# Optimization experiments

Hardware: AMD Instinct MI355X
Metric: run time of the kernel (lower is better)

## Reference

```python
import jax, jax.numpy as jnp
import numpy as np

DIM = 1024
HEADS = 16
HEAD_DIM = DIM // HEADS


def setup_inputs() -> dict:
    key = jax.random.key(0)
    ks = jax.random.split(key, 5)
    s = 1.0 / np.sqrt(DIM)
    x = jax.random.normal(ks[0], (2, 2048, DIM), dtype=jnp.float32)
    # torch nn.Linear weights are [out_features, in_features]
    W_qkv = jax.random.uniform(ks[1], (3 * DIM, DIM), dtype=jnp.float32, minval=-s, maxval=s)
    b_qkv = jax.random.uniform(ks[2], (3 * DIM,), dtype=jnp.float32, minval=-s, maxval=s)
    W_out = jax.random.uniform(ks[3], (DIM, DIM), dtype=jnp.float32, minval=-s, maxval=s)
    b_out = jax.random.uniform(ks[4], (DIM,), dtype=jnp.float32, minval=-s, maxval=s)
    return {"x": x, "W_qkv": W_qkv, "b_qkv": b_qkv, "W_out": W_out, "b_out": b_out}


def reference(x, W_qkv, b_qkv, W_out, b_out):
    B, N, D = x.shape
    qkv = jnp.einsum('bnd,ed->bne', x, W_qkv) + b_qkv            # [B,N,3D]
    qkv = qkv.reshape(B, N, 3, HEADS, HEAD_DIM)
    qkv = jnp.transpose(qkv, (2, 0, 3, 1, 4))                    # [3,B,H,N,hd]
    q, k, v = qkv[0], qkv[1], qkv[2]
    scale = 1.0 / np.sqrt(HEAD_DIM).astype(np.float32)
    attn = jnp.einsum('bhnd,bhmd->bhnm', q, k) * scale           # [B,H,N,N]
    attn = jax.nn.softmax(attn, axis=-1)
    out = jnp.einsum('bhnm,bhmd->bhnd', attn, v)                 # [B,H,N,hd]
    out = jnp.transpose(out, (0, 2, 1, 3)).reshape(B, N, D)
    out = jnp.einsum('bnd,ed->bne', out, W_out) + b_out
    return out
```

## Files before the change

kernel.cpp:

```cpp
#include <hip/hip_runtime.h>
#include <stdint.h>
#include <stddef.h>

typedef __attribute__((ext_vector_type(4))) float  f32x4;
typedef __attribute__((ext_vector_type(8))) short  s16x8;
typedef __attribute__((ext_vector_type(4))) float  float4v;
typedef __attribute__((ext_vector_type(4))) unsigned short u16x4;
typedef __attribute__((ext_vector_type(2))) unsigned int   u32x2;

#define DIM    1024
#define HEADS  16
#define HD     64
#define SEQ    2048
#define BATCH  2
#define TOKENS (BATCH * SEQ)

#define QSCALE 0.18033688011112042f

__device__ __forceinline__ unsigned short f2bf(float f) {
  union { float f; uint32_t u; } x; x.f = f;
  uint32_t r = x.u + 0x7fffu + ((x.u >> 16) & 1u);
  return (unsigned short)(r >> 16);
}

__device__ __forceinline__ float fast_exp2(float x) {
#if __has_builtin(__builtin_amdgcn_exp2f)
  return __builtin_amdgcn_exp2f(x);
#else
  return exp2f(x);
#endif
}

__device__ __forceinline__ uint32_t pack_bf16_trunc(uint32_t lo, uint32_t hi) {
#if __has_builtin(__builtin_amdgcn_perm)
  return __builtin_amdgcn_perm(hi, lo, 0x07060302u);
#else
  return (hi & 0xffff0000u) | (lo >> 16);
#endif
}

__device__ __forceinline__ void stage16(const unsigned short* gp, unsigned short* lp) {
#if __has_builtin(__builtin_amdgcn_global_load_lds)
  __builtin_amdgcn_global_load_lds((const __attribute__((address_space(1))) void*)gp,
                                   (__attribute__((address_space(3))) void*)lp, 16, 0, 0);
#else
  *(s16x8*)(lp + (threadIdx.x & 63) * 8) = *(const s16x8*)gp;
#endif
}

#define N4_X  (TOKENS * DIM / 4)
#define N4_WQ (3 * DIM * DIM / 4)
#define N4_WO (DIM * DIM / 4)
__global__ __launch_bounds__(256) void mhsa_cast_all(const float* __restrict__ x,
    const float* __restrict__ wq, const float* __restrict__ wo,
    unsigned short* __restrict__ xb, unsigned short* __restrict__ wqb,
    unsigned short* __restrict__ wob) {
  int i = blockIdx.x * 256 + threadIdx.x;
  const float* src; unsigned short* dst; int off;
  if (i < N4_X)              { src = x;  dst = xb;  off = i; }
  else if (i < N4_X + N4_WQ) { src = wq; dst = wqb; off = i - N4_X; }
  else                       { src = wo; dst = wob; off = i - (N4_X + N4_WQ); }
  float4v f = ((const float4v*)src)[off];
  u16x4 o;
  o.x = f2bf(f.x); o.y = f2bf(f.y); o.z = f2bf(f.z); o.w = f2bf(f.w);
  ((u16x4*)dst)[off] = o;
}


__global__ __launch_bounds__(256, 3) void mhsa_gemm_qkv(const unsigned short* __restrict__ A,
    const unsigned short* __restrict__ Bw, const float* __restrict__ bias,
    unsigned short* __restrict__ qws, unsigned short* __restrict__ kws,
    unsigned short* __restrict__ vws) {
  __shared__ unsigned short As[2][128 * 32];
  __shared__ unsigned short Bs[2][128 * 32];
  const int t = threadIdx.x;
  const int w = t >> 6, l = t & 63;
  const int wm = w >> 1, wn = w & 1;
  const int rowBase = blockIdx.y * 128;
  const int colBase = blockIdx.x * 128;
  const int fr = l & 15, q4 = l >> 4, ln = l & 15;
  const int srow = l >> 2;
  const int scol = ((l & 3) ^ (srow & 3)) * 8;

  f32x4 zero = {0.f, 0.f, 0.f, 0.f};
  f32x4 acc[4][4];
  #pragma unroll
  for (int a = 0; a < 4; ++a)
    #pragma unroll
    for (int b = 0; b < 4; ++b) acc[a][b] = zero;

  #pragma unroll
  for (int it = 0; it < 2; ++it) {
    const int c = w * 2 + it;
    stage16(A  + (size_t)(rowBase + c * 16 + srow) * DIM + scol, &As[0][c * 512]);
    stage16(Bw + (size_t)(colBase + c * 16 + srow) * DIM + scol, &Bs[0][c * 512]);
  }
  __syncthreads();

  for (int kt = 0; kt < DIM / 32; ++kt) {
    const int cur = kt & 1, nxt = cur ^ 1;
    if (kt + 1 < DIM / 32) {
      const int k1 = (kt + 1) * 32;
      #pragma unroll
      for (int it = 0; it < 2; ++it) {
        const int c = w * 2 + it;
        stage16(A  + (size_t)(rowBase + c * 16 + srow) * DIM + k1 + scol, &As[nxt][c * 512]);
        stage16(Bw + (size_t)(colBase + c * 16 + srow) * DIM + k1 + scol, &Bs[nxt][c * 512]);
      }
    }
    s16x8 xf[4], wf[4];
    #pragma unroll
    for (int b = 0; b < 4; ++b)
      xf[b] = *(const s16x8*)&As[cur][(wm * 64 + b * 16 + fr) * 32 + ((q4 ^ (fr & 3)) * 8)];
    #pragma unroll
    for (int a = 0; a < 4; ++a)
      wf[a] = *(const s16x8*)&Bs[cur][(wn * 64 + a * 16 + fr) * 32 + ((q4 ^ (fr & 3)) * 8)];
    #pragma unroll
    for (int a = 0; a < 4; ++a)
      #pragma unroll
      for (int b = 0; b < 4; ++b)
        acc[a][b] = __builtin_amdgcn_mfma_f32_16x16x32_bf16(wf[a], xf[b], acc[a][b], 0, 0, 0);
    __syncthreads();
  }

  const int which = colBase >> 10;
  const float sc = (which == 0) ? QSCALE : 1.0f;
  unsigned short* dst = (which == 0) ? qws : ((which == 1) ? kws : vws);

  #pragma unroll
  for (int a = 0; a < 4; ++a) {
    const int e0 = colBase + wn * 64 + a * 16 + q4 * 4;
    const float4v bs4 = *(const float4v*)&bias[e0];
    const int rr0 = e0 & 1023;
    const int h = rr0 >> 6, d0 = rr0 & 63;
    #pragma unroll
    for (int b = 0; b < 4; ++b) {
      const int tok = rowBase + wm * 64 + b * 16 + ln;
      const int bb = tok >> 11, n = tok & 2047;
      if (which != 2) {
        u16x4 pk;
        #pragma unroll
        for (int r = 0; r < 4; ++r) pk[r] = f2bf((acc[a][b][r] + bs4[r]) * sc);
        *(u16x4*)&dst[(((size_t)(bb * HEADS + h)) * SEQ + n) * HD + d0] = pk;
      } else {
        #pragma unroll
        for (int r = 0; r < 4; ++r)
          dst[(((size_t)(bb * HEADS + h)) * HD + d0 + r) * SEQ + n] =
              f2bf(acc[a][b][r] + bs4[r]);
      }
    }
  }
}

__global__ __launch_bounds__(256, 3) void mhsa_gemm_out(const unsigned short* __restrict__ A,
    const unsigned short* __restrict__ Bw, const float* __restrict__ bias,
    float* __restrict__ out) {
  __shared__ unsigned short As[2][64 * 32];
  __shared__ unsigned short Bs[2][128 * 32];
  const int t = threadIdx.x;
  const int w = t >> 6, l = t & 63;
  const int wm = w >> 1, wn = w & 1;
  const int rowBase = blockIdx.y * 64;
  const int colBase = blockIdx.x * 128;
  const int fr = l & 15, q4 = l >> 4, ln = l & 15;
  const int srow = l >> 2;
  const int scol = ((l & 3) ^ (srow & 3)) * 8;

  f32x4 zero = {0.f, 0.f, 0.f, 0.f};
  f32x4 acc[4][2];
  #pragma unroll
  for (int a = 0; a < 4; ++a)
    #pragma unroll
    for (int b = 0; b < 2; ++b) acc[a][b] = zero;

  #pragma unroll
  for (int it = 0; it < 3; ++it) {
    const int s = w * 3 + it;
    if (s < 4) stage16(A  + (size_t)(rowBase + s * 16 + srow) * DIM + scol, &As[0][s * 512]);
    else       stage16(Bw + (size_t)(colBase + (s - 4) * 16 + srow) * DIM + scol, &Bs[0][(s - 4) * 512]);
  }
  __syncthreads();

  for (int kt = 0; kt < DIM / 32; ++kt) {
    const int cur = kt & 1, nxt = cur ^ 1;
    if (kt + 1 < DIM / 32) {
      const int k1 = (kt + 1) * 32;
      #pragma unroll
      for (int it = 0; it < 3; ++it) {
        const int s = w * 3 + it;
        if (s < 4) stage16(A  + (size_t)(rowBase + s * 16 + srow) * DIM + k1 + scol, &As[nxt][s * 512]);
        else       stage16(Bw + (size_t)(colBase + (s - 4) * 16 + srow) * DIM + k1 + scol, &Bs[nxt][(s - 4) * 512]);
      }
    }
    s16x8 xf[2], wf[4];
    #pragma unroll
    for (int b = 0; b < 2; ++b)
      xf[b] = *(const s16x8*)&As[cur][(wm * 32 + b * 16 + fr) * 32 + ((q4 ^ (fr & 3)) * 8)];
    #pragma unroll
    for (int a = 0; a < 4; ++a)
      wf[a] = *(const s16x8*)&Bs[cur][(wn * 64 + a * 16 + fr) * 32 + ((q4 ^ (fr & 3)) * 8)];
    #pragma unroll
    for (int a = 0; a < 4; ++a)
      #pragma unroll
      for (int b = 0; b < 2; ++b)
        acc[a][b] = __builtin_amdgcn_mfma_f32_16x16x32_bf16(wf[a], xf[b], acc[a][b], 0, 0, 0);
    __syncthreads();
  }

  #pragma unroll
  for (int a = 0; a < 4; ++a) {
    const int e0 = colBase + wn * 64 + a * 16 + q4 * 4;
    const float4v bs4 = *(const float4v*)&bias[e0];
    #pragma unroll
    for (int b = 0; b < 2; ++b) {
      const int tok = rowBase + wm * 32 + b * 16 + ln;
      float4v v;
      #pragma unroll
      for (int r = 0; r < 4; ++r) v[r] = acc[a][b][r] + bs4[r];
      *(float4v*)&out[(size_t)tok * DIM + e0] = v;
    }
  }
}

__global__ __launch_bounds__(256, 2) void mhsa_attn(const unsigned short* __restrict__ q,
    const unsigned short* __restrict__ k, const unsigned short* __restrict__ vt,
    unsigned short* __restrict__ o) {
  __shared__ unsigned short QPs[4 * 32 * 72];
  __shared__ unsigned short Ks[2][64 * 64];
  __shared__ unsigned short Vs[2][64 * 64];
  const int t = threadIdx.x, w = t >> 6, l = t & 63;
  const int q4 = l >> 4, ln = l & 15;
  const int bh = blockIdx.y, q0 = blockIdx.x * 128;
  const unsigned short* qb  = q  + (size_t)bh * SEQ * HD;
  const unsigned short* kb  = k  + (size_t)bh * SEQ * HD;
  const unsigned short* vtb = vt + (size_t)bh * HD * SEQ;

  const int srow = l >> 3;
  const int scol = ((l & 7) ^ srow) * 8;

  unsigned short* Pw = &QPs[w * (32 * 72)];

  #pragma unroll
  for (int it = 0; it < 4; ++it)
    stage16(qb + (size_t)(q0 + w * 32 + it * 8 + srow) * HD + scol, &Pw[it * 512]);
  #pragma unroll
  for (int it = 0; it < 2; ++it) {
    const int c = w + it * 4;
    stage16(kb  + (size_t)(c * 8 + srow) * HD + scol,        &Ks[0][c * 512]);
    stage16(vtb + (size_t)(c * 8 + srow) * SEQ + scol,       &Vs[0][c * 512]);
    stage16(kb  + (size_t)(64 + c * 8 + srow) * HD + scol,   &Ks[1][c * 512]);
  }
  __syncthreads();

  s16x8 aq[2][2];
  #pragma unroll
  for (int i = 0; i < 2; ++i)
    #pragma unroll
    for (int kk = 0; kk < 2; ++kk)
      aq[i][kk] = *(const s16x8*)&Pw[(i * 16 + ln) * 64 + (((kk * 4 + q4) ^ (ln & 7)) * 8)];

  f32x4 zero = {0.f, 0.f, 0.f, 0.f};
  f32x4 accO[2][4];
  float lsum[2] = {0.f, 0.f};
  #pragma unroll
  for (int i = 0; i < 2; ++i)
    #pragma unroll
    for (int jd = 0; jd < 4; ++jd) accO[i][jd] = zero;

  {
    f32x4 St[4][2];
    #pragma unroll
    for (int jb = 0; jb < 4; ++jb)
      #pragma unroll
      for (int i = 0; i < 2; ++i) St[jb][i] = zero;
    #pragma unroll
    for (int jb = 0; jb < 4; ++jb) {
      s16x8 ak0 = *(const s16x8*)&Ks[0][(jb * 16 + ln) * 64 + ((q4 ^ (ln & 7)) * 8)];
      s16x8 ak1 = *(const s16x8*)&Ks[0][(jb * 16 + ln) * 64 + (((4 + q4) ^ (ln & 7)) * 8)];
      #pragma unroll
      for (int i = 0; i < 2; ++i) {
        St[jb][i] = __builtin_amdgcn_mfma_f32_16x16x32_bf16(ak0, aq[i][0], St[jb][i], 0, 0, 0);
        St[jb][i] = __builtin_amdgcn_mfma_f32_16x16x32_bf16(ak1, aq[i][1], St[jb][i], 0, 0, 0);
      }
    }
    #pragma unroll
    for (int i = 0; i < 2; ++i)
      #pragma unroll
      for (int jb = 0; jb < 4; ++jb) {
        uint32_t u0 = __float_as_uint(fast_exp2(St[jb][i][0]));
        uint32_t u1 = __float_as_uint(fast_exp2(St[jb][i][1]));
        uint32_t u2 = __float_as_uint(fast_exp2(St[jb][i][2]));
        uint32_t u3 = __float_as_uint(fast_exp2(St[jb][i][3]));
        lsum[i] += __uint_as_float(u0 & 0xffff0000u) + __uint_as_float(u1 & 0xffff0000u)
                 + __uint_as_float(u2 & 0xffff0000u) + __uint_as_float(u3 & 0xffff0000u);
        u32x2 pk;
        pk.x = pack_bf16_trunc(u0, u1);
        pk.y = pack_bf16_trunc(u2, u3);
        *(u32x2*)&Pw[(i * 16 + ln) * 72 + jb * 16 + q4 * 4] = pk;
      }
  }
  __syncthreads();

  const int NT = SEQ / 64;
  for (int jt = 0; jt < NT; ++jt) {
    const int cur = jt & 1, nxt = cur ^ 1;
    if (jt + 2 < NT) {
      const int j2 = (jt + 2) * 64;
      #pragma unroll
      for (int it = 0; it < 2; ++it) {
        const int c = w + it * 4;
        stage16(kb + (size_t)(j2 + c * 8 + srow) * HD + scol, &Ks[cur][c * 512]);
      }
    }
    if (jt + 1 < NT) {
      const int j1 = (jt + 1) * 64;
      #pragma unroll
      for (int it = 0; it < 2; ++it) {
        const int c = w + it * 4;
        stage16(vtb + (size_t)(c * 8 + srow) * SEQ + j1 + scol, &Vs[nxt][c * 512]);
      }
    }

    s16x8 ap[2][2];
    #pragma unroll
    for (int i = 0; i < 2; ++i)
      #pragma unroll
      for (int kk = 0; kk < 2; ++kk)
        ap[i][kk] = *(const s16x8*)&Pw[(i * 16 + ln) * 72 + kk * 32 + q4 * 8];

    if (jt + 1 < NT) {
      f32x4 St[4][2];
      #pragma unroll
      for (int jb = 0; jb < 4; ++jb)
        #pragma unroll
        for (int i = 0; i < 2; ++i) St[jb][i] = zero;
      #pragma unroll
      for (int jb = 0; jb < 4; ++jb) {
        s16x8 ak0 = *(const s16x8*)&Ks[nxt][(jb * 16 + ln) * 64 + ((q4 ^ (ln & 7)) * 8)];
        s16x8 ak1 = *(const s16x8*)&Ks[nxt][(jb * 16 + ln) * 64 + (((4 + q4) ^ (ln & 7)) * 8)];
        #pragma unroll
        for (int i = 0; i < 2; ++i) {
          St[jb][i] = __builtin_amdgcn_mfma_f32_16x16x32_bf16(ak0, aq[i][0], St[jb][i], 0, 0, 0);
          St[jb][i] = __builtin_amdgcn_mfma_f32_16x16x32_bf16(ak1, aq[i][1], St[jb][i], 0, 0, 0);
        }
      }

      #pragma unroll
      for (int jd = 0; jd < 4; ++jd) {
        s16x8 bv0 = *(const s16x8*)&Vs[cur][(jd * 16 + ln) * 64 + ((q4 ^ (ln & 7)) * 8)];
        s16x8 bv1 = *(const s16x8*)&Vs[cur][(jd * 16 + ln) * 64 + (((4 + q4) ^ (ln & 7)) * 8)];
        #pragma unroll
        for (int i = 0; i < 2; ++i) {
          accO[i][jd] = __builtin_amdgcn_mfma_f32_16x16x32_bf16(ap[i][0], bv0, accO[i][jd], 0, 0, 0);
          accO[i][jd] = __builtin_amdgcn_mfma_f32_16x16x32_bf16(ap[i][1], bv1, accO[i][jd], 0, 0, 0);
        }
      }

      #pragma unroll
      for (int i = 0; i < 2; ++i)
        #pragma unroll
        for (int jb = 0; jb < 4; ++jb) {
          uint32_t u0 = __float_as_uint(fast_exp2(St[jb][i][0]));
          uint32_t u1 = __float_as_uint(fast_exp2(St[jb][i][1]));
          uint32_t u2 = __float_as_uint(fast_exp2(St[jb][i][2]));
          uint32_t u3 = __float_as_uint(fast_exp2(St[jb][i][3]));
          lsum[i] += __uint_as_float(u0 & 0xffff0000u) + __uint_as_float(u1 & 0xffff0000u)
                   + __uint_as_float(u2 & 0xffff0000u) + __uint_as_float(u3 & 0xffff0000u);
          u32x2 pk;
          pk.x = pack_bf16_trunc(u0, u1);
          pk.y = pack_bf16_trunc(u2, u3);
          *(u32x2*)&Pw[(i * 16 + ln) * 72 + jb * 16 + q4 * 4] = pk;
        }
    } else {
      #pragma unroll
      for (int jd = 0; jd < 4; ++jd) {
        s16x8 bv0 = *(const s16x8*)&Vs[cur][(jd * 16 + ln) * 64 + ((q4 ^ (ln & 7)) * 8)];
        s16x8 bv1 = *(const s16x8*)&Vs[cur][(jd * 16 + ln) * 64 + (((4 + q4) ^ (ln & 7)) * 8)];
        #pragma unroll
        for (int i = 0; i < 2; ++i) {
          accO[i][jd] = __builtin_amdgcn_mfma_f32_16x16x32_bf16(ap[i][0], bv0, accO[i][jd], 0, 0, 0);
          accO[i][jd] = __builtin_amdgcn_mfma_f32_16x16x32_bf16(ap[i][1], bv1, accO[i][jd], 0, 0, 0);
        }
      }
    }

    __syncthreads();
  }

  const int b = bh >> 4, h = bh & 15;
  #pragma unroll
  for (int i = 0; i < 2; ++i) {
    float s = lsum[i];
    s += __shfl_xor(s, 16);
    s += __shfl_xor(s, 32);
    const float inv = 1.f / s;
    #pragma unroll
    for (int r = 0; r < 4; ++r) {
      const float invr = __shfl(inv, (l & 48) + q4 * 4 + r);
      const int row = q0 + w * 32 + i * 16 + q4 * 4 + r;
      #pragma unroll
      for (int jd = 0; jd < 4; ++jd)
        o[((size_t)(b * SEQ + row)) * DIM + h * HD + jd * 16 + ln] = f2bf(accO[i][jd][r] * invr);
    }
  }
}

extern "C" void kernel_launch(void* const* d_in, const int* in_sizes, int n_in,
                              void* d_out, int out_size, void* d_ws, size_t ws_size,
                              hipStream_t stream) {
  const float* x     = (const float*)d_in[0];
  const float* Wqkv  = (const float*)d_in[1];
  const float* bqkv  = (const float*)d_in[2];
  const float* Wout  = (const float*)d_in[3];
  const float* bout  = (const float*)d_in[4];
  float* out = (float*)d_out;

  unsigned short* ws = (unsigned short*)d_ws;
  unsigned short* x_bf    = ws;
  unsigned short* wqkv_bf = x_bf    + (size_t)TOKENS * DIM;
  unsigned short* wout_bf = wqkv_bf + (size_t)3 * DIM * DIM;
  unsigned short* q_ws    = wout_bf + (size_t)DIM * DIM;
  unsigned short* k_ws    = q_ws    + (size_t)TOKENS * DIM;
  unsigned short* v_ws    = k_ws    + (size_t)TOKENS * DIM;
  unsigned short* ao_ws   = v_ws    + (size_t)TOKENS * DIM;

  {
    const int n4 = N4_X + N4_WQ + N4_WO;
    mhsa_cast_all<<<n4 / 256, 256, 0, stream>>>(x, Wqkv, Wout, x_bf, wqkv_bf, wout_bf);
  }

  {
    dim3 grid(3 * DIM / 128, TOKENS / 128);
    mhsa_gemm_qkv<<<grid, 256, 0, stream>>>(x_bf, wqkv_bf, bqkv, q_ws, k_ws, v_ws);
  }

  {
    dim3 grid(SEQ / 128, BATCH * HEADS);
    mhsa_attn<<<grid, 256, 0, stream>>>(q_ws, k_ws, v_ws, ao_ws);
  }

  {
    dim3 grid(DIM / 128, TOKENS / 64);
    mhsa_gemm_out<<<grid, 256, 0, stream>>>(ao_ws, wout_bf, bout, out);
  }
}
```

Baseline: 193.1 us.

## Store Q/K/V in MFMA fragment order and load fragments directly from global

The QKV projection epilogue now writes Q, K and V in a pre-swizzled layout that matches the MFMA operand fragments. The attention kernel can then load each lane's 8-element fragment straight from global memory into registers. This drops the shared-memory staging of K and V and the per-tile __syncthreads, with register double-buffering of K and V fragments replacing the LDS double-buffering. The cost is higher register pressure from 64 extra VGPRs of fragment buffers. It also relies on L2/global latency being hidden without LDS reuse, since each wave reloads K/V independently (four waves read the same data), and the V epilogue now uses scattered 2-byte stores.

```diff
diff --git a/kernel.cpp b/kernel.cpp
--- a/kernel.cpp
+++ b/kernel.cpp
@@ -124,29 +124,47 @@
   }
 
   const int which = colBase >> 10;
-  const float sc = (which == 0) ? QSCALE : 1.0f;
-  unsigned short* dst = (which == 0) ? qws : ((which == 1) ? kws : vws);
-
-  #pragma unroll
-  for (int a = 0; a < 4; ++a) {
-    const int e0 = colBase + wn * 64 + a * 16 + q4 * 4;
-    const float4v bs4 = *(const float4v*)&bias[e0];
-    const int rr0 = e0 & 1023;
-    const int h = rr0 >> 6, d0 = rr0 & 63;
-    #pragma unroll
-    for (int b = 0; b < 4; ++b) {
-      const int tok = rowBase + wm * 64 + b * 16 + ln;
-      const int bb = tok >> 11, n = tok & 2047;
-      if (which != 2) {
+  if (which != 2) {
+    unsigned short* dst = (which == 0) ? qws : kws;
+    const float sc = (which == 0) ? QSCALE : 1.0f;
+    #pragma unroll
+    for (int a = 0; a < 4; ++a) {
+      const int e0 = colBase + wn * 64 + a * 16 + q4 * 4;
+      const float4v bs4 = *(const float4v*)&bias[e0];
+      const int h = (e0 & 1023) >> 6;
+      const int kkf = a >> 1;
+      const int q4s = ((a & 1) << 1) | (q4 >> 1);
+      const int jf  = (q4 & 1) * 4;
+      #pragma unroll
+      for (int b = 0; b < 4; ++b) {
+        const int tok = rowBase + wm * 64 + b * 16 + ln;
+        const int bb = tok >> 11, n = tok & 2047;
+        const int bhl = bb * HEADS + h;
         u16x4 pk;
         #pragma unroll
         for (int r = 0; r < 4; ++r) pk[r] = f2bf((acc[a][b][r] + bs4[r]) * sc);
-        *(u16x4*)&dst[(((size_t)(bb * HEADS + h)) * SEQ + n) * HD + d0] = pk;
-      } else {
+        const size_t off = ((size_t)(bhl * (SEQ / 16) + (n >> 4)) * 2 + kkf) * 512
+                         + q4s * 128 + ln * 8 + jf;
+        *(u16x4*)&dst[off] = pk;
+      }
+    }
+  } else {
+    #pragma unroll
+    for (int a = 0; a < 4; ++a) {
+      const int e0 = colBase + wn * 64 + a * 16 + q4 * 4;
+      const float4v bs4 = *(const float4v*)&bias[e0];
+      const int h = (e0 & 1023) >> 6;
+      #pragma unroll
+      for (int b = 0; b < 4; ++b) {
+        const int tok = rowBase + wm * 64 + b * 16 + ln;
+        const int bb = tok >> 11, n = tok & 2047;
+        const int bhl = bb * HEADS + h;
+        const int kt = n >> 6, kkf = (n >> 5) & 1, q4s = (n >> 3) & 3, jf = n & 7;
+        const size_t base = ((size_t)((bhl * (SEQ / 64) + kt) * 8 + a * 2 + kkf)) * 512
+                          + q4s * 128 + jf;
         #pragma unroll
         for (int r = 0; r < 4; ++r)
-          dst[(((size_t)(bb * HEADS + h)) * HD + d0 + r) * SEQ + n] =
-              f2bf(acc[a][b][r] + bs4[r]);
+          vws[base + (q4 * 4 + r) * 8] = f2bf(acc[a][b][r] + bs4[r]);
       }
     }
   }
@@ -222,42 +240,24 @@
   }
 }
 
-__global__ __launch_bounds__(256, 2) void mhsa_attn(const unsigned short* __restrict__ q,
-    const unsigned short* __restrict__ k, const unsigned short* __restrict__ vt,
+__global__ __launch_bounds__(256, 2) void mhsa_attn(const unsigned short* __restrict__ qF,
+    const unsigned short* __restrict__ kF, const unsigned short* __restrict__ vF,
     unsigned short* __restrict__ o) {
-  __shared__ unsigned short QPs[4 * 32 * 72];
-  __shared__ unsigned short Ks[2][64 * 64];
-  __shared__ unsigned short Vs[2][64 * 64];
+  __shared__ unsigned short Ps[4 * 32 * 72];
   const int t = threadIdx.x, w = t >> 6, l = t & 63;
   const int q4 = l >> 4, ln = l & 15;
   const int bh = blockIdx.y, q0 = blockIdx.x * 128;
-  const unsigned short* qb  = q  + (size_t)bh * SEQ * HD;
-  const unsigned short* kb  = k  + (size_t)bh * SEQ * HD;
-  const unsigned short* vtb = vt + (size_t)bh * HD * SEQ;
-
-  const int srow = l >> 3;
-  const int scol = ((l & 7) ^ srow) * 8;
-
-  unsigned short* Pw = &QPs[w * (32 * 72)];
-
-  #pragma unroll
-  for (int it = 0; it < 4; ++it)
-    stage16(qb + (size_t)(q0 + w * 32 + it * 8 + srow) * HD + scol, &Pw[it * 512]);
-  #pragma unroll
-  for (int it = 0; it < 2; ++it) {
-    const int c = w + it * 4;
-    stage16(kb  + (size_t)(c * 8 + srow) * HD + scol,        &Ks[0][c * 512]);
-    stage16(vtb + (size_t)(c * 8 + srow) * SEQ + scol,       &Vs[0][c * 512]);
-    stage16(kb  + (size_t)(64 + c * 8 + srow) * HD + scol,   &Ks[1][c * 512]);
-  }
-  __syncthreads();
+  const unsigned short* qb = qF + (size_t)bh * (SEQ * HD);
+  const unsigned short* kb = kF + (size_t)bh * (SEQ * HD);
+  const unsigned short* vb = vF + (size_t)bh * (SEQ * HD);
+  unsigned short* Pw = &Ps[w * (32 * 72)];
 
   s16x8 aq[2][2];
   #pragma unroll
   for (int i = 0; i < 2; ++i)
     #pragma unroll
     for (int kk = 0; kk < 2; ++kk)
-      aq[i][kk] = *(const s16x8*)&Pw[(i * 16 + ln) * 64 + (((kk * 4 + q4) ^ (ln & 7)) * 8)];
+      aq[i][kk] = *(const s16x8*)&qb[((size_t)((q0 >> 4) + w * 2 + i) * 2 + kk) * 512 + l * 8];
 
   f32x4 zero = {0.f, 0.f, 0.f, 0.f};
   f32x4 accO[2][4];
@@ -267,6 +267,17 @@
     #pragma unroll
     for (int jd = 0; jd < 4; ++jd) accO[i][jd] = zero;
 
+  s16x8 kfr[2][4][2], vfr[2][4][2];
+
+  #pragma unroll
+  for (int jb = 0; jb < 4; ++jb)
+    #pragma unroll
+    for (int kk = 0; kk < 2; ++kk) {
+      kfr[1][jb][kk] = *(const s16x8*)&kb[(size_t)((jb * 2 + kk)) * 512 + l * 8];
+      vfr[0][jb][kk] = *(const s16x8*)&vb[(size_t)((jb * 2 + kk)) * 512 + l * 8];
+      kfr[0][jb][kk] = *(const s16x8*)&kb[(size_t)(((4 + jb) * 2 + kk)) * 512 + l * 8];
+    }
+
   {
     f32x4 St[4][2];
     #pragma unroll
@@ -274,15 +285,12 @@
       #pragma unroll
       for (int i = 0; i < 2; ++i) St[jb][i] = zero;
     #pragma unroll
-    for (int jb = 0; jb < 4; ++jb) {
-      s16x8 ak0 = *(const s16x8*)&Ks[0][(jb * 16 + ln) * 64 + ((q4 ^ (ln & 7)) * 8)];
-      s16x8 ak1 = *(const s16x8*)&Ks[0][(jb * 16 + ln) * 64 + (((4 + q4) ^ (ln & 7)) * 8)];
+    for (int jb = 0; jb < 4; ++jb)
       #pragma unroll
       for (int i = 0; i < 2; ++i) {
-        St[jb][i] = __builtin_amdgcn_mfma_f32_16x16x32_bf16(ak0, aq[i][0], St[jb][i], 0, 0, 0);
-        St[jb][i] = __builtin_amdgcn_mfma_f32_16x16x32_bf16(ak1, aq[i][1], St[jb][i], 0, 0, 0);
-      }
-    }
+        St[jb][i] = __builtin_amdgcn_mfma_f32_16x16x32_bf16(kfr[1][jb][0], aq[i][0], St[jb][i], 0, 0, 0);
+        St[jb][i] = __builtin_amdgcn_mfma_f32_16x16x32_bf16(kfr[1][jb][1], aq[i][1], St[jb][i], 0, 0, 0);
+      }
     #pragma unroll
     for (int i = 0; i < 2; ++i)
       #pragma unroll
@@ -299,26 +307,23 @@
         *(u32x2*)&Pw[(i * 16 + ln) * 72 + jb * 16 + q4 * 4] = pk;
       }
   }
-  __syncthreads();
 
   const int NT = SEQ / 64;
   for (int jt = 0; jt < NT; ++jt) {
-    const int cur = jt & 1, nxt = cur ^ 1;
+    const int p = jt & 1, pn = p ^ 1;
     if (jt + 2 < NT) {
-      const int j2 = (jt + 2) * 64;
-      #pragma unroll
-      for (int it = 0; it < 2; ++it) {
-        const int c = w + it * 4;
-        stage16(kb + (size_t)(j2 + c * 8 + srow) * HD + scol, &Ks[cur][c * 512]);
-      }
+      #pragma unroll
+      for (int jb = 0; jb < 4; ++jb)
+        #pragma unroll
+        for (int kk = 0; kk < 2; ++kk)
+          kfr[pn][jb][kk] = *(const s16x8*)&kb[(size_t)(((jt + 2) * 4 + jb) * 2 + kk) * 512 + l * 8];
     }
     if (jt + 1 < NT) {
-      const int j1 = (jt + 1) * 64;
-      #pragma unroll
-      for (int it = 0; it < 2; ++it) {
-        const int c = w + it * 4;
-        stage16(vtb + (size_t)(c * 8 + srow) * SEQ + j1 + scol, &Vs[nxt][c * 512]);
-      }
+      #pragma unroll
+      for (int jb = 0; jb < 4; ++jb)
+        #pragma unroll
+        for (int kk = 0; kk < 2; ++kk)
+          vfr[pn][jb][kk] = *(const s16x8*)&vb[(size_t)((jt + 1) * 8 + jb * 2 + kk) * 512 + l * 8];
     }
 
     s16x8 ap[2][2];
@@ -335,26 +340,20 @@
         #pragma unroll
         for (int i = 0; i < 2; ++i) St[jb][i] = zero;
       #pragma unroll
-      for (int jb = 0; jb < 4; ++jb) {
-        s16x8 ak0 = *(const s16x8*)&Ks[nxt][(jb * 16 + ln) * 64 + ((q4 ^ (ln & 7)) * 8)];
-        s16x8 ak1 = *(const s16x8*)&Ks[nxt][(jb * 16 + ln) * 64 + (((4 + q4) ^ (ln & 7)) * 8)];
+      for (int jb = 0; jb < 4; ++jb)
         #pragma unroll
         for (int i = 0; i < 2; ++i) {
-          St[jb][i] = __builtin_amdgcn_mfma_f32_16x16x32_bf16(ak0, aq[i][0], St[jb][i], 0, 0, 0);
-          St[jb][i] = __builtin_amdgcn_mfma_f32_16x16x32_bf16(ak1, aq[i][1], St[jb][i], 0, 0, 0);
+          St[jb][i] = __builtin_amdgcn_mfma_f32_16x16x32_bf16(kfr[p][jb][0], aq[i][0], St[jb][i], 0, 0, 0);
+          St[jb][i] = __builtin_amdgcn_mfma_f32_16x16x32_bf16(kfr[p][jb][1], aq[i][1], St[jb][i], 0, 0, 0);
         }
-      }
-
-      #pragma unroll
-      for (int jd = 0; jd < 4; ++jd) {
-        s16x8 bv0 = *(const s16x8*)&Vs[cur][(jd * 16 + ln) * 64 + ((q4 ^ (ln & 7)) * 8)];
-        s16x8 bv1 = *(const s16x8*)&Vs[cur][(jd * 16 + ln) * 64 + (((4 + q4) ^ (ln & 7)) * 8)];
+
+      #pragma unroll
+      for (int jd = 0; jd < 4; ++jd)
         #pragma unroll
         for (int i = 0; i < 2; ++i) {
-          accO[i][jd] = __builtin_amdgcn_mfma_f32_16x16x32_bf16(ap[i][0], bv0, accO[i][jd], 0, 0, 0);
-          accO[i][jd] = __builtin_amdgcn_mfma_f32_16x16x32_bf16(ap[i][1], bv1, accO[i][jd], 0, 0, 0);
+          accO[i][jd] = __builtin_amdgcn_mfma_f32_16x16x32_bf16(ap[i][0], vfr[p][jd][0], accO[i][jd], 0, 0, 0);
+          accO[i][jd] = __builtin_amdgcn_mfma_f32_16x16x32_bf16(ap[i][1], vfr[p][jd][1], accO[i][jd], 0, 0, 0);
         }
-      }
 
       #pragma unroll
       for (int i = 0; i < 2; ++i)
@@ -373,18 +372,13 @@
         }
     } else {
       #pragma unroll
-      for (int jd = 0; jd < 4; ++jd) {
-        s16x8 bv0 = *(const s16x8*)&Vs[cur][(jd * 16 + ln) * 64 + ((q4 ^ (ln & 7)) * 8)];
-        s16x8 bv1 = *(const s16x8*)&Vs[cur][(jd * 16 + ln) * 64 + (((4 + q4) ^ (ln & 7)) * 8)];
+      for (int jd = 0; jd < 4; ++jd)
         #pragma unroll
         for (int i = 0; i < 2; ++i) {
-          accO[i][jd] = __builtin_amdgcn_mfma_f32_16x16x32_bf16(ap[i][0], bv0, accO[i][jd], 0, 0, 0);
-          accO[i][jd] = __builtin_amdgcn_mfma_f32_16x16x32_bf16(ap[i][1], bv1, accO[i][jd], 0, 0, 0);
+          accO[i][jd] = __builtin_amdgcn_mfma_f32_16x16x32_bf16(ap[i][0], vfr[p][jd][0], accO[i][jd], 0, 0, 0);
+          accO[i][jd] = __builtin_amdgcn_mfma_f32_16x16x32_bf16(ap[i][1], vfr[p][jd][1], accO[i][jd], 0, 0, 0);
         }
-      }
-    }
-
-    __syncthreads();
+    }
   }
 
   const int b = bh >> 4, h = bh & 15;
```

After: 463.8 us. 2.4x slower.
